# Kernel tuning notes

Measured on AMD Instinct MI355X. Metric: run time of the kernel, lower is better.

The kernel has to match this reference:

```python
import jax, jax.numpy as jnp
import numpy as np

B, L, C, OUT = 8, 256, 512, 512


def setup_inputs() -> dict:
    key = jax.random.key(0)
    ks = jax.random.split(key, 8)
    xd = jax.random.normal(ks[0], (B, L, C), jnp.float32)
    xt = jax.random.normal(ks[1], (B, L, C), jnp.float32)
    # Linear weights stored (in, out): y = x @ W + b (equiv. to torch x @ W^T)
    Wc = jax.random.normal(ks[2], (C, C), jnp.float32) * 0.02
    bc = jnp.zeros((C,), jnp.float32)
    Wp = jax.random.normal(ks[3], (C, C), jnp.float32) * 0.02
    bp = jnp.zeros((C,), jnp.float32)
    Wf = jax.random.normal(ks[4], (C, OUT), jnp.float32) * 0.02
    bf = jnp.zeros((OUT,), jnp.float32)
    return {"xd": xd, "xt": xt, "Wc": Wc, "bc": bc, "Wp": Wp, "bp": bp, "Wf": Wf, "bf": bf}


def reference(xd, xt, Wc, bc, Wp, bp, Wf, bf):
    # projected features
    pt = jax.nn.relu(xt) @ Wp + bp              # (b, Lt, C)
    pc = jax.nn.relu(xd) @ Wc + bc              # (b, Ld, C)
    # sigmoid bilinear scores: (b, Lt, Ld) == (b, Ld, Lt) since Lt == Ld structurally
    scores = jax.nn.sigmoid(jnp.einsum('bic,bkc->bik', pt, pc))
    # normalize by total per-batch sum
    w = scores / jnp.sum(scores, axis=(1, 2), keepdims=True)
    # tanh of elementwise outer product, reduced with attention weights
    # cp[b,c] = sum_{i,j} tanh(xd[b,i,c] * xt[b,j,c]) * w[b,i,j]
    cp = jnp.einsum('bijc,bij->bc', jnp.tanh(xd[:, :, None, :] * xt[:, None, :, :]), w)
    return cp @ Wf + bf
```

## Files before the change

kernel.cpp:

```cpp
#include <hip/hip_runtime.h>
#include <math.h>

#define B_   8
#define L_   256
#define C_   512
#define OUT_ 512

typedef _Float16 half8 __attribute__((ext_vector_type(8)));
typedef _Float16 half4 __attribute__((ext_vector_type(4)));
typedef float    f32x4 __attribute__((ext_vector_type(4)));

__global__ __launch_bounds__(256)
void wconv_kernel(const float* __restrict__ Wp, const float* __restrict__ Wc,
                  _Float16* __restrict__ hWp, _Float16* __restrict__ hWc)
{
    const int which = blockIdx.z;
    const float* __restrict__ W = which ? Wc : Wp;
    _Float16* __restrict__ H    = which ? hWc : hWp;
    __shared__ float tl[32][33];
    const int k0 = blockIdx.y << 5, n0 = blockIdx.x << 5;
    const int tr = threadIdx.x >> 5, tc = threadIdx.x & 31;
    #pragma unroll
    for (int i = 0; i < 32; i += 8)
        tl[tr + i][tc] = W[(size_t)(k0 + tr + i) * C_ + n0 + tc];
    __syncthreads();
    #pragma unroll
    for (int i = 0; i < 32; i += 8)
        H[(size_t)(n0 + tr + i) * C_ + k0 + tc] = (_Float16)tl[tc][tr + i];
}

__global__ __launch_bounds__(256)
void proj_mfma_kernel(const float* __restrict__ xt, const _Float16* __restrict__ hWp,
                      const float* __restrict__ bp,
                      const float* __restrict__ xd, const _Float16* __restrict__ hWc,
                      const float* __restrict__ bc,
                      _Float16* __restrict__ pt, _Float16* __restrict__ pc)
{
    const int which = blockIdx.z;
    const float*    __restrict__ X    = which ? xd : xt;
    const _Float16* __restrict__ W    = which ? hWc : hWp;
    const float*    __restrict__ bias = which ? bc : bp;
    _Float16*       __restrict__ Y    = which ? pc : pt;

    __shared__ _Float16 Ah[2][64][40];
    __shared__ _Float16 Bh[2][64][40];
    __shared__ _Float16 Ot[64][72];

    const int tid = threadIdx.x;
    const int m0 = blockIdx.y << 6, n0 = blockIdx.x << 6;
    const int srow = tid >> 2, sch = (tid & 3) << 3;
    const int lane = tid & 63, wv = tid >> 6;
    const int l15 = lane & 15, quad = lane >> 4;

    const float*    Ag = X + (size_t)(m0 + srow) * C_ + sch;
    const _Float16* Bg = W + (size_t)(n0 + srow) * C_ + sch;

    float4 a0 = *(const float4*)(Ag);
    float4 a1 = *(const float4*)(Ag + 4);
    half8  bv = *(const half8*)(Bg);

    {
        half8 av;
        av[0] = (_Float16)fmaxf(a0.x, 0.f); av[1] = (_Float16)fmaxf(a0.y, 0.f);
        av[2] = (_Float16)fmaxf(a0.z, 0.f); av[3] = (_Float16)fmaxf(a0.w, 0.f);
        av[4] = (_Float16)fmaxf(a1.x, 0.f); av[5] = (_Float16)fmaxf(a1.y, 0.f);
        av[6] = (_Float16)fmaxf(a1.z, 0.f); av[7] = (_Float16)fmaxf(a1.w, 0.f);
        *(half8*)&Ah[0][srow][sch] = av;
        *(half8*)&Bh[0][srow][sch] = bv;
    }

    f32x4 acc[4] = {};
    for (int ks = 0; ks < 16; ++ks) {
        const int cur = ks & 1;
        if (ks < 15) {
            Ag += 32; Bg += 32;
            a0 = *(const float4*)(Ag);
            a1 = *(const float4*)(Ag + 4);
            bv = *(const half8*)(Bg);
        }
        __syncthreads();
        half8 af = *(const half8*)&Ah[cur][(wv << 4) + l15][quad << 3];
        #pragma unroll
        for (int nb = 0; nb < 4; ++nb) {
            half8 bf = *(const half8*)&Bh[cur][(nb << 4) + l15][quad << 3];
            acc[nb] = __builtin_amdgcn_mfma_f32_16x16x32_f16(af, bf, acc[nb], 0, 0, 0);
        }
        if (ks < 15) {
            half8 av;
            av[0] = (_Float16)fmaxf(a0.x, 0.f); av[1] = (_Float16)fmaxf(a0.y, 0.f);
            av[2] = (_Float16)fmaxf(a0.z, 0.f); av[3] = (_Float16)fmaxf(a0.w, 0.f);
            av[4] = (_Float16)fmaxf(a1.x, 0.f); av[5] = (_Float16)fmaxf(a1.y, 0.f);
            av[6] = (_Float16)fmaxf(a1.z, 0.f); av[7] = (_Float16)fmaxf(a1.w, 0.f);
            *(half8*)&Ah[cur ^ 1][srow][sch] = av;
            *(half8*)&Bh[cur ^ 1][srow][sch] = bv;
        }
    }

    __syncthreads();
    #pragma unroll
    for (int nb = 0; nb < 4; ++nb) {
        const float bz = bias[n0 + (nb << 4) + l15];
        #pragma unroll
        for (int r = 0; r < 4; ++r)
            Ot[(wv << 4) + (quad << 2) + r][(nb << 4) + l15] = (_Float16)(acc[nb][r] + bz);
    }
    __syncthreads();
    const int erow = tid >> 3, ech = (tid & 7) << 3;
    #pragma unroll
    for (int h = 0; h < 64; h += 32)
        *(half8*)&Y[(size_t)(m0 + erow + h) * C_ + n0 + ech] = *(const half8*)&Ot[erow + h][ech];
}

__device__ __forceinline__ float sigmoid_fast(float z) {
    float e = __builtin_amdgcn_exp2f(-1.4426950408889634f * z);
    return __builtin_amdgcn_rcpf(e + 1.0f);
}

__global__ __launch_bounds__(512, 4)
void cp_scores_kernel(const _Float16* __restrict__ pt, const _Float16* __restrict__ pc,
                      const float* __restrict__ xd, const float* __restrict__ xt,
                      float* __restrict__ partials, float* __restrict__ sums_part)
{
    const int bx = blockIdx.x, by = blockIdx.y, b = blockIdx.z;
    const int i0 = bx << 5, j0 = by << 5;
    const int tid = threadIdx.x;
    const int lane = tid & 63, wv = tid >> 6;
    const int l15 = lane & 15, quad = lane >> 4;

    __shared__ _Float16 Ah[2][32][40];
    __shared__ _Float16 Bh[2][32][40];
    __shared__ float ws_[32][36];
    __shared__ float wred[4];

    const int sHalf = tid >> 8;
    const int srow  = (tid & 255) >> 3;
    const int sch   = (tid & 7) << 2;
    const _Float16* Sg = (sHalf ? pc + (size_t)(b * L_ + j0 + srow) * C_
                                : pt + (size_t)(b * L_ + i0 + srow) * C_) + sch;

    half4 v = *(const half4*)Sg;
    if (sHalf) *(half4*)&Bh[0][srow][sch] = v; else *(half4*)&Ah[0][srow][sch] = v;

    f32x4 acc = {};
    for (int ks = 0; ks < 16; ++ks) {
        const int cur = ks & 1;
        if (ks < 15) { Sg += 32; v = *(const half4*)Sg; }
        __syncthreads();
        if (wv < 4) {
            half8 af = *(const half8*)&Ah[cur][((wv >> 1) << 4) + l15][quad << 3];
            half8 bf = *(const half8*)&Bh[cur][((wv & 1) << 4) + l15][quad << 3];
            acc = __builtin_amdgcn_mfma_f32_16x16x32_f16(af, bf, acc, 0, 0, 0);
        }
        if (ks < 15) {
            if (sHalf) *(half4*)&Bh[cur ^ 1][srow][sch] = v;
            else       *(half4*)&Ah[cur ^ 1][srow][sch] = v;
        }
    }

    float lsum = 0.f;
    if (wv < 4) {
        const int n = ((wv & 1) << 4) + l15;
        const int m = ((wv >> 1) << 4) + (quad << 2);
        float4 sg;
        sg.x = sigmoid_fast(acc[0]);
        sg.y = sigmoid_fast(acc[1]);
        sg.z = sigmoid_fast(acc[2]);
        sg.w = sigmoid_fast(acc[3]);
        *(float4*)&ws_[n][m] = sg;
        lsum = (sg.x + sg.y) + (sg.z + sg.w);
    }
    #pragma unroll
    for (int off = 32; off; off >>= 1) lsum += __shfl_xor(lsum, off);
    if (wv < 4 && lane == 0) wred[wv] = lsum;
    __syncthreads();
    if (tid == 0)
        sums_part[(b << 6) | (bx << 3) | by] = (wred[0] + wred[1]) + (wred[2] + wred[3]);

    const int c = tid;
    const float* __restrict__ xdb = xd + (size_t)(b * L_ + i0) * C_ + c;
    const float* __restrict__ xtb = xt + (size_t)(b * L_ + j0) * C_ + c;
    float xds[32], xtv[32];
    #pragma unroll
    for (int i = 0; i < 32; ++i)
        xds[i] = xdb[(size_t)i * C_] * 2.8853900817779268f;
    #pragma unroll
    for (int j = 0; j < 32; ++j)
        xtv[j] = xtb[(size_t)j * C_];

    float a0 = 0.f, a1 = 0.f, a2 = 0.f, a3 = 0.f;
    for (int jj = 0; jj < 32; ++jj) {
        const float xv = xtv[jj];
        #pragma unroll
        for (int i = 0; i < 32; i += 4) {
            const float4 w4 = *(const float4*)&ws_[jj][i];
            float e0 = __builtin_amdgcn_exp2f(xds[i + 0] * xv);
            float e1 = __builtin_amdgcn_exp2f(xds[i + 1] * xv);
            float q0 = e0 + 1.0f, q1 = e1 + 1.0f;
            float rp01 = __builtin_amdgcn_rcpf(q0 * q1);
            a0 = fmaf(w4.x, rp01 * q1, a0);
            a1 = fmaf(w4.y, rp01 * q0, a1);
            float e2 = __builtin_amdgcn_exp2f(xds[i + 2] * xv);
            float e3 = __builtin_amdgcn_exp2f(xds[i + 3] * xv);
            float q2 = e2 + 1.0f, q3 = e3 + 1.0f;
            float rp23 = __builtin_amdgcn_rcpf(q2 * q3);
            a2 = fmaf(w4.z, rp23 * q3, a2);
            a3 = fmaf(w4.w, rp23 * q2, a3);
        }
    }
    const int p = (bx << 3) | by;
    partials[(size_t)((b << 6) | p) * C_ + c] = (a0 + a1) + (a2 + a3);
}

__global__ __launch_bounds__(512)
void finalize_kernel(const float* __restrict__ partials, const float* __restrict__ sums_part,
                     const float* __restrict__ Wf, const float* __restrict__ bfv,
                     float* __restrict__ out)
{
    const int b = blockIdx.y;
    const int t = threadIdx.x;
    __shared__ float cp[C_];
    __shared__ float red[512];
    __shared__ float sumsh;

    red[t] = (t < 64) ? sums_part[(b << 6) | t] : 0.f;

    float s = 0.f;
    #pragma unroll
    for (int p = 0; p < 64; ++p)
        s += partials[(size_t)((b << 6) | p) * C_ + t];

    __syncthreads();
    for (int st = 256; st > 0; st >>= 1) {
        if (t < st) red[t] += red[t + st];
        __syncthreads();
    }
    if (t == 0) sumsh = red[0];
    __syncthreads();

    cp[t] = 1.0f - 2.0f * s / sumsh;
    __syncthreads();

    const int o  = ((int)blockIdx.x << 6) | (t & 63);
    const int c0 = (t >> 6) << 6;
    float acc = 0.f;
    #pragma unroll 8
    for (int i = 0; i < 64; ++i) {
        const int cc = c0 + i;
        acc = fmaf(cp[cc], Wf[(size_t)cc * OUT_ + o], acc);
    }
    red[t] = acc;
    __syncthreads();
    if (t < 64) {
        float a = 0.f;
        #pragma unroll
        for (int g = 0; g < 8; ++g) a += red[(g << 6) | t];
        out[(size_t)b * OUT_ + o] = a + bfv[o];
    }
}

extern "C" void kernel_launch(void* const* d_in, const int* in_sizes, int n_in,
                              void* d_out, int out_size, void* d_ws, size_t ws_size,
                              hipStream_t stream)
{
    const float* xd = (const float*)d_in[0];
    const float* xt = (const float*)d_in[1];
    const float* Wc = (const float*)d_in[2];
    const float* bc = (const float*)d_in[3];
    const float* Wp = (const float*)d_in[4];
    const float* bp = (const float*)d_in[5];
    const float* Wf = (const float*)d_in[6];
    const float* bf = (const float*)d_in[7];
    float* out = (float*)d_out;

    _Float16* hWp = (_Float16*)d_ws;
    _Float16* hWc = hWp + 262144;
    _Float16* pt  = hWc + 262144;
    _Float16* pc  = pt + 1048576;
    float* partials  = (float*)(pc + 1048576);
    float* sums_part = partials + B_ * 64 * C_;

    wconv_kernel<<<dim3(16, 16, 2), 256, 0, stream>>>(Wp, Wc, hWp, hWc);
    proj_mfma_kernel<<<dim3(8, 32, 2), 256, 0, stream>>>(xt, hWp, bp, xd, hWc, bc, pt, pc);
    cp_scores_kernel<<<dim3(8, 8, 8), 512, 0, stream>>>(pt, pc, xd, xt, partials, sums_part);
    finalize_kernel<<<dim3(8, 8), 512, 0, stream>>>(partials, sums_part, Wf, bf, out);
}
```

Before: 147.9 us.

## Fuse weight transpose into projection GEMM and pack tanh loop as float2

Removes the separate weight transpose/convert kernel. The projection kernel now loads fp32 weights column-wise (coalesced across n) and converts them to half on the fly into the transposed shared-memory layout. This saves one launch and a workspace round trip, at the cost of more global loads per thread (8 scalar loads instead of one half8). The tanh-weighted reduction loop is also rewritten with float2 vectors so the compiler can emit packed FP32 multiply/FMA instructions.

```diff
diff --git a/kernel.cpp b/kernel.cpp
--- a/kernel.cpp
+++ b/kernel.cpp
@@ -9,38 +9,20 @@
 typedef _Float16 half8 __attribute__((ext_vector_type(8)));
 typedef _Float16 half4 __attribute__((ext_vector_type(4)));
 typedef float    f32x4 __attribute__((ext_vector_type(4)));
+typedef float    f32x2 __attribute__((ext_vector_type(2)));
 
 __global__ __launch_bounds__(256)
-void wconv_kernel(const float* __restrict__ Wp, const float* __restrict__ Wc,
-                  _Float16* __restrict__ hWp, _Float16* __restrict__ hWc)
-{
-    const int which = blockIdx.z;
-    const float* __restrict__ W = which ? Wc : Wp;
-    _Float16* __restrict__ H    = which ? hWc : hWp;
-    __shared__ float tl[32][33];
-    const int k0 = blockIdx.y << 5, n0 = blockIdx.x << 5;
-    const int tr = threadIdx.x >> 5, tc = threadIdx.x & 31;
-    #pragma unroll
-    for (int i = 0; i < 32; i += 8)
-        tl[tr + i][tc] = W[(size_t)(k0 + tr + i) * C_ + n0 + tc];
-    __syncthreads();
-    #pragma unroll
-    for (int i = 0; i < 32; i += 8)
-        H[(size_t)(n0 + tr + i) * C_ + k0 + tc] = (_Float16)tl[tc][tr + i];
-}
-
-__global__ __launch_bounds__(256)
-void proj_mfma_kernel(const float* __restrict__ xt, const _Float16* __restrict__ hWp,
+void proj_mfma_kernel(const float* __restrict__ xt, const float* __restrict__ Wp,
                       const float* __restrict__ bp,
-                      const float* __restrict__ xd, const _Float16* __restrict__ hWc,
+                      const float* __restrict__ xd, const float* __restrict__ Wc,
                       const float* __restrict__ bc,
                       _Float16* __restrict__ pt, _Float16* __restrict__ pc)
 {
     const int which = blockIdx.z;
-    const float*    __restrict__ X    = which ? xd : xt;
-    const _Float16* __restrict__ W    = which ? hWc : hWp;
-    const float*    __restrict__ bias = which ? bc : bp;
-    _Float16*       __restrict__ Y    = which ? pc : pt;
+    const float* __restrict__ X    = which ? xd : xt;
+    const float* __restrict__ W    = which ? Wc : Wp;
+    const float* __restrict__ bias = which ? bc : bp;
+    _Float16*    __restrict__ Y    = which ? pc : pt;
 
     __shared__ _Float16 Ah[2][64][40];
     __shared__ _Float16 Bh[2][64][40];
@@ -48,16 +30,19 @@
 
     const int tid = threadIdx.x;
     const int m0 = blockIdx.y << 6, n0 = blockIdx.x << 6;
-    const int srow = tid >> 2, sch = (tid & 3) << 3;
     const int lane = tid & 63, wv = tid >> 6;
     const int l15 = lane & 15, quad = lane >> 4;
 
-    const float*    Ag = X + (size_t)(m0 + srow) * C_ + sch;
-    const _Float16* Bg = W + (size_t)(n0 + srow) * C_ + sch;
+    const int srow = tid >> 2, sch = (tid & 3) << 3;
+    const float* Ag = X + (size_t)(m0 + srow) * C_ + sch;
+    const int nl = tid & 63, kseg = tid >> 6;
+    const float* Bg = W + (size_t)(kseg << 3) * C_ + n0 + nl;
 
     float4 a0 = *(const float4*)(Ag);
     float4 a1 = *(const float4*)(Ag + 4);
-    half8  bv = *(const half8*)(Bg);
+    float wr[8];
+    #pragma unroll
+    for (int r = 0; r < 8; ++r) wr[r] = Bg[(size_t)r * C_];
 
     {
         half8 av;
@@ -66,17 +51,22 @@
         av[4] = (_Float16)fmaxf(a1.x, 0.f); av[5] = (_Float16)fmaxf(a1.y, 0.f);
         av[6] = (_Float16)fmaxf(a1.z, 0.f); av[7] = (_Float16)fmaxf(a1.w, 0.f);
         *(half8*)&Ah[0][srow][sch] = av;
-        *(half8*)&Bh[0][srow][sch] = bv;
+        half8 bv;
+        #pragma unroll
+        for (int r = 0; r < 8; ++r) bv[r] = (_Float16)wr[r];
+        *(half8*)&Bh[0][nl][kseg << 3] = bv;
     }
 
     f32x4 acc[4] = {};
     for (int ks = 0; ks < 16; ++ks) {
         const int cur = ks & 1;
         if (ks < 15) {
-            Ag += 32; Bg += 32;
+            Ag += 32;
+            Bg += 32 * C_;
             a0 = *(const float4*)(Ag);
             a1 = *(const float4*)(Ag + 4);
-            bv = *(const half8*)(Bg);
+            #pragma unroll
+            for (int r = 0; r < 8; ++r) wr[r] = Bg[(size_t)r * C_];
         }
         __syncthreads();
         half8 af = *(const half8*)&Ah[cur][(wv << 4) + l15][quad << 3];
@@ -92,7 +82,10 @@
             av[4] = (_Float16)fmaxf(a1.x, 0.f); av[5] = (_Float16)fmaxf(a1.y, 0.f);
             av[6] = (_Float16)fmaxf(a1.z, 0.f); av[7] = (_Float16)fmaxf(a1.w, 0.f);
             *(half8*)&Ah[cur ^ 1][srow][sch] = av;
-            *(half8*)&Bh[cur ^ 1][srow][sch] = bv;
+            half8 bv;
+            #pragma unroll
+            for (int r = 0; r < 8; ++r) bv[r] = (_Float16)wr[r];
+            *(half8*)&Bh[cur ^ 1][nl][kseg << 3] = bv;
         }
     }
 
@@ -179,36 +172,42 @@
     const int c = tid;
     const float* __restrict__ xdb = xd + (size_t)(b * L_ + i0) * C_ + c;
     const float* __restrict__ xtb = xt + (size_t)(b * L_ + j0) * C_ + c;
-    float xds[32], xtv[32];
-    #pragma unroll
-    for (int i = 0; i < 32; ++i)
-        xds[i] = xdb[(size_t)i * C_] * 2.8853900817779268f;
+    f32x2 xds2[16];
+    float xtv[32];
+    #pragma unroll
+    for (int i = 0; i < 16; ++i) {
+        xds2[i].x = xdb[(size_t)(2 * i) * C_]     * 2.8853900817779268f;
+        xds2[i].y = xdb[(size_t)(2 * i + 1) * C_] * 2.8853900817779268f;
+    }
     #pragma unroll
     for (int j = 0; j < 32; ++j)
         xtv[j] = xtb[(size_t)j * C_];
 
-    float a0 = 0.f, a1 = 0.f, a2 = 0.f, a3 = 0.f;
+    f32x2 acc01 = {0.f, 0.f}, acc23 = {0.f, 0.f};
     for (int jj = 0; jj < 32; ++jj) {
         const float xv = xtv[jj];
         #pragma unroll
         for (int i = 0; i < 32; i += 4) {
             const float4 w4 = *(const float4*)&ws_[jj][i];
-            float e0 = __builtin_amdgcn_exp2f(xds[i + 0] * xv);
-            float e1 = __builtin_amdgcn_exp2f(xds[i + 1] * xv);
-            float q0 = e0 + 1.0f, q1 = e1 + 1.0f;
-            float rp01 = __builtin_amdgcn_rcpf(q0 * q1);
-            a0 = fmaf(w4.x, rp01 * q1, a0);
-            a1 = fmaf(w4.y, rp01 * q0, a1);
-            float e2 = __builtin_amdgcn_exp2f(xds[i + 2] * xv);
-            float e3 = __builtin_amdgcn_exp2f(xds[i + 3] * xv);
-            float q2 = e2 + 1.0f, q3 = e3 + 1.0f;
-            float rp23 = __builtin_amdgcn_rcpf(q2 * q3);
-            a2 = fmaf(w4.z, rp23 * q3, a2);
-            a3 = fmaf(w4.w, rp23 * q2, a3);
+            f32x2 x01 = xds2[i >> 1] * xv;
+            f32x2 e01 = { __builtin_amdgcn_exp2f(x01.x), __builtin_amdgcn_exp2f(x01.y) };
+            f32x2 q01 = e01 + 1.0f;
+            float rp01 = __builtin_amdgcn_rcpf(q01.x * q01.y);
+            f32x2 r01 = rp01 * __builtin_shufflevector(q01, q01, 1, 0);
+            f32x2 w01 = { w4.x, w4.y };
+            acc01 = w01 * r01 + acc01;
+            f32x2 x23 = xds2[(i >> 1) + 1] * xv;
+            f32x2 e23 = { __builtin_amdgcn_exp2f(x23.x), __builtin_amdgcn_exp2f(x23.y) };
+            f32x2 q23 = e23 + 1.0f;
+            float rp23 = __builtin_amdgcn_rcpf(q23.x * q23.y);
+            f32x2 r23 = rp23 * __builtin_shufflevector(q23, q23, 1, 0);
+            f32x2 w23 = { w4.z, w4.w };
+            acc23 = w23 * r23 + acc23;
         }
     }
     const int p = (bx << 3) | by;
-    partials[(size_t)((b << 6) | p) * C_ + c] = (a0 + a1) + (a2 + a3);
+    partials[(size_t)((b << 6) | p) * C_ + c] =
+        (acc01.x + acc01.y) + (acc23.x + acc23.y);
 }
 
 __global__ __launch_bounds__(512)
@@ -272,15 +271,12 @@
     const float* bf = (const float*)d_in[7];
     float* out = (float*)d_out;
 
-    _Float16* hWp = (_Float16*)d_ws;
-    _Float16* hWc = hWp + 262144;
-    _Float16* pt  = hWc + 262144;
+    _Float16* pt  = (_Float16*)d_ws;
     _Float16* pc  = pt + 1048576;
     float* partials  = (float*)(pc + 1048576);
     float* sums_part = partials + B_ * 64 * C_;
 
-    wconv_kernel<<<dim3(16, 16, 2), 256, 0, stream>>>(Wp, Wc, hWp, hWc);
-    proj_mfma_kernel<<<dim3(8, 32, 2), 256, 0, stream>>>(xt, hWp, bp, xd, hWc, bc, pt, pc);
+    proj_mfma_kernel<<<dim3(8, 32, 2), 256, 0, stream>>>(xt, Wp, bp, xd, Wc, bc, pt, pc);
     cp_scores_kernel<<<dim3(8, 8, 8), 512, 0, stream>>>(pt, pc, xd, xt, partials, sums_part);
     finalize_kernel<<<dim3(8, 8), 512, 0, stream>>>(partials, sums_part, Wf, bf, out);
 }
```

After: 139.3 us. 5.9% less time.
